# Kernel tuning notes

Measured on AMD Instinct MI355X. Metric: run time of the kernel, lower is better.

Reference implementation:

```python
import jax, jax.numpy as jnp
import numpy as np

C_S, C_Z, H = 384, 128, 8
HD = C_S // H
EPS = 1e-5

def _layernorm(x, g, b):
    mu = jnp.mean(x, axis=-1, keepdims=True)
    var = jnp.mean((x - mu) ** 2, axis=-1, keepdims=True)
    return (x - mu) * jax.lax.rsqrt(var + EPS) * g + b

def setup_inputs() -> dict:
    key = jax.random.key(0)
    ks = jax.random.split(key, 12)
    B, L = 1, 768
    sc = lambda d: 1.0 / np.sqrt(d)
    return {
        "single": jax.random.normal(ks[0], (B, L, C_S), jnp.float32),
        "pair": jax.random.normal(ks[1], (B, L, L, C_Z), jnp.float32),
        "g_s": jnp.ones((C_S,), jnp.float32),
        "b_s": jnp.zeros((C_S,), jnp.float32),
        "g_z": jnp.ones((C_Z,), jnp.float32),
        "b_z": jnp.zeros((C_Z,), jnp.float32),
        "Wq": jax.random.normal(ks[2], (C_S, C_S), jnp.float32) * sc(C_S),
        "Wk": jax.random.normal(ks[3], (C_S, C_S), jnp.float32) * sc(C_S),
        "Wv": jax.random.normal(ks[4], (C_S, C_S), jnp.float32) * sc(C_S),
        "Wb": jax.random.normal(ks[5], (C_Z, H), jnp.float32) * sc(C_Z),
        "Wo": jax.random.normal(ks[6], (C_S, C_S), jnp.float32) * sc(C_S),
        "bo": jnp.zeros((C_S,), jnp.float32),
        "Wg": jax.random.normal(ks[7], (C_S, C_S), jnp.float32) * sc(C_S),
        "bg": jnp.zeros((C_S,), jnp.float32),
    }

def reference(single, pair, g_s, b_s, g_z, b_z, Wq, Wk, Wv, Wb, Wo, bo, Wg, bg):
    B, L, _ = single.shape
    s = _layernorm(single, g_s, b_s)                      # [B,L,C_S]
    z = _layernorm(pair, g_z, b_z)                        # [B,L,L,C_Z]
    q = (s @ Wq.T).reshape(B, L, H, HD)
    k = (s @ Wk.T).reshape(B, L, H, HD)
    v = (s @ Wv.T).reshape(B, L, H, HD)
    attn = jnp.einsum('bihd,bjhd->bhij', q, k) / np.sqrt(HD)
    bias = jnp.einsum('bijz,zh->bhij', z, Wb)             # pair bias per head
    attn = jax.nn.softmax(attn + bias, axis=-1)
    out = jnp.einsum('bhij,bjhd->bihd', attn, v).reshape(B, L, C_S)
    gate = jax.nn.sigmoid(s @ Wg.T + bg)
    return single + gate * (out @ Wo.T + bo)
```

## Files before the change

### kernel.cpp

```cpp
#include <hip/hip_runtime.h>
#include <hip/hip_bf16.h>
#include <cstdint>
#include <cstddef>

#define LSEQ 768
#define CS 384
#define CZ 128
#define NH 8
#define HD 48
#define LL (LSEQ*LSEQ)
#define WELEM 147456

static constexpr float EPS = 1e-5f;
static constexpr float QK_SCALE = 0.14433756729740643f;

typedef unsigned short u16;
typedef __attribute__((ext_vector_type(8))) short bf16x8;
typedef __attribute__((ext_vector_type(4))) float f32x4;

__device__ __forceinline__ u16 f2bf_s(float f){
  unsigned int u = __float_as_uint(f);
  unsigned int r = u + 0x7fffu + ((u >> 16) & 1u);
  return (u16)(r >> 16);
}

__global__ __launch_bounds__(256) void k_prep(
    const float* __restrict__ single,
    const float* __restrict__ g, const float* __restrict__ b,
    const float* __restrict__ Wq, const float* __restrict__ Wk,
    const float* __restrict__ Wv, const float* __restrict__ Wg,
    const float* __restrict__ Wo,
    u16* __restrict__ s_bf, u16* __restrict__ Wbf){
  const int blk = blockIdx.x;
  if(blk < 192){
    const int wave = threadIdx.x >> 6, lane = threadIdx.x & 63;
    const int i = blk*4 + wave;
    const float* row = single + i*CS;
    float x[6];
    float sum = 0.f;
#pragma unroll
    for(int e=0;e<6;e++){ x[e] = row[lane + 64*e]; sum += x[e]; }
#pragma unroll
    for(int m=32;m>=1;m>>=1) sum += __shfl_xor(sum, m, 64);
    const float mu = sum * (1.f/CS);
    float vs = 0.f;
#pragma unroll
    for(int e=0;e<6;e++){ float d = x[e]-mu; vs += d*d; }
#pragma unroll
    for(int m=32;m>=1;m>>=1) vs += __shfl_xor(vs, m, 64);
    const float rs = rsqrtf(vs*(1.f/CS) + EPS);
#pragma unroll
    for(int e=0;e<6;e++){
      int c = lane + 64*e;
      s_bf[i*CS + c] = f2bf_s((x[e]-mu)*rs*g[c] + b[c]);
    }
  } else {
    const int idx = (blk-192)*256 + threadIdx.x;
    const int which = idx / 36864;
    const int off = (idx - which*36864)*4;
    const float* src = (which==0)?Wq:(which==1)?Wk:(which==2)?Wv:(which==3)?Wg:Wo;
    const float4 u = *(const float4*)(src + off);
    ushort4 o;
    o.x = f2bf_s(u.x); o.y = f2bf_s(u.y); o.z = f2bf_s(u.z); o.w = f2bf_s(u.w);
    *(ushort4*)(Wbf + (size_t)which*WELEM + off) = o;
  }
}

#define NQKVG 288
#define NPAIR 3072
__global__ __launch_bounds__(256,4) void k_pair_qkvg(
    const float* __restrict__ pair,
    const float* __restrict__ g_z,
    const float* __restrict__ b_z,
    const float* __restrict__ Wb,
    float* __restrict__ bias,
    const u16* __restrict__ s_bf, const u16* __restrict__ Wbf,
    const float* __restrict__ bg,
    u16* __restrict__ qb, u16* __restrict__ kb,
    u16* __restrict__ vT, float* __restrict__ gate){
  const int t = threadIdx.x;
  const int lane = t & 63;

  if(blockIdx.x < NQKVG){
    const int blk = blockIdx.x;
    const int w = t >> 6, ln = lane & 15, quad = lane >> 4;
    const int bx = blk % 12, by = blk / 12;
    const int m0 = bx*64 + w*16;
    const int which = by / 6;
    const int n0 = (by % 6)*64;
    const u16* W = Wbf + (size_t)which*WELEM;

    const u16* arow = s_bf + (size_t)(m0+ln)*CS + quad*8;
    const u16* brow = W + (size_t)(n0+ln)*CS + quad*8;

    f32x4 acc[4];
#pragma unroll
    for(int nb=0;nb<4;nb++) acc[nb] = (f32x4){0.f,0.f,0.f,0.f};

#pragma unroll 2
    for(int k0=0;k0<CS;k0+=32){
      bf16x8 a = *(const bf16x8*)(arow + k0);
#pragma unroll
      for(int nb=0;nb<4;nb++){
        bf16x8 bb = *(const bf16x8*)(brow + (size_t)nb*16*CS + k0);
        acc[nb] = __builtin_amdgcn_mfma_f32_16x16x32_bf16(a, bb, acc[nb], 0,0,0);
      }
    }

    if(which == 2){
#pragma unroll
      for(int nb=0;nb<4;nb++){
        const int col = n0 + nb*16 + ln;
        ushort4 sv;
        sv.x = f2bf_s(acc[nb][0]); sv.y = f2bf_s(acc[nb][1]);
        sv.z = f2bf_s(acc[nb][2]); sv.w = f2bf_s(acc[nb][3]);
        *(ushort4*)(vT + (size_t)col*LSEQ + m0 + quad*4) = sv;
      }
    } else {
#pragma unroll
      for(int nb=0;nb<4;nb++){
#pragma unroll
        for(int r=0;r<4;r++){
          const int row = m0 + quad*4 + r;
          const int col = n0 + nb*16 + ln;
          const float val = acc[nb][r];
          if(which==0)      qb[row*CS+col] = f2bf_s(val*QK_SCALE);
          else if(which==1) kb[row*CS+col] = f2bf_s(val);
          else              gate[row*CS+col] = 1.f/(1.f + __expf(-(val + bg[col])));
        }
      }
    }
    return;
  }

  const int wave = t >> 6;
  const int sub  = lane >> 4;
  const int lg   = lane & 15;
  const int z0   = lg*8;

  float wb_r[64], gz[8], bz[8];
#pragma unroll
  for(int zz=0; zz<8; zz++){
    gz[zz] = g_z[z0+zz];
    bz[zz] = b_z[z0+zz];
#pragma unroll
    for(int h=0; h<NH; h++) wb_r[zz*8+h] = Wb[(z0+zz)*NH + h];
  }
  const int hmap = 4*(lg&1) + (lg&2) + ((lg>>2)&1);

  const int ngroups = LL/16;
  for(int gidx = blockIdx.x - NQKVG; gidx < ngroups; gidx += NPAIR){
    const int r = gidx*16 + wave*4 + sub;
    const float4 u0 = *(const float4*)(pair + (size_t)r*CZ + z0);
    const float4 u1 = *(const float4*)(pair + (size_t)r*CZ + z0 + 4);
    float x[8] = {u0.x,u0.y,u0.z,u0.w,u1.x,u1.y,u1.z,u1.w};
    float sum=0.f, sq=0.f;
#pragma unroll
    for(int e=0;e<8;e++){ sum += x[e]; sq += x[e]*x[e]; }
#pragma unroll
    for(int m=1;m<16;m<<=1){ sum += __shfl_xor(sum,m,64); sq += __shfl_xor(sq,m,64); }
    const float mu = sum*(1.f/CZ);
    const float rs = rsqrtf(sq*(1.f/CZ) - mu*mu + EPS);
    float acc[8];
#pragma unroll
    for(int h=0;h<8;h++) acc[h]=0.f;
#pragma unroll
    for(int e=0;e<8;e++){
      const float zn = (x[e]-mu)*rs*gz[e] + bz[e];
#pragma unroll
      for(int h=0;h<8;h++) acc[h] += zn*wb_r[e*8+h];
    }
    float k1[4];
    {
      const bool hi = lg & 1;
#pragma unroll
      for(int j=0;j<4;j++){
        float send = hi ? acc[j] : acc[j+4];
        float recv = __shfl_xor(send, 1, 64);
        k1[j] = (hi ? acc[j+4] : acc[j]) + recv;
      }
    }
    float k2[2];
    {
      const bool hi = lg & 2;
#pragma unroll
      for(int j=0;j<2;j++){
        float send = hi ? k1[j] : k1[j+2];
        float recv = __shfl_xor(send, 2, 64);
        k2[j] = (hi ? k1[j+2] : k1[j]) + recv;
      }
    }
    float k3;
    {
      const bool hi = lg & 4;
      float send = hi ? k2[0] : k2[1];
      float recv = __shfl_xor(send, 4, 64);
      k3 = (hi ? k2[1] : k2[0]) + recv;
    }
    k3 += __shfl_xor(k3, 8, 64);
    if(lg < 8) bias[(size_t)hmap*LL + r] = k3;
  }
}

__global__ __launch_bounds__(256) void k_flash(
    const u16* __restrict__ qb, const u16* __restrict__ kb,
    const u16* __restrict__ vT, const float* __restrict__ bias,
    u16* __restrict__ attno_bf){
  const int h  = blockIdx.y;
  const int i0 = blockIdx.x * 16;
  const int t  = threadIdx.x;
  const int w    = t >> 6;
  const int lane = t & 63;
  const int ln   = lane & 15;
  const int quad = lane >> 4;

  __shared__ u16  S_lds[4][16][32];
  __shared__ float O_lds[4][16][48];
  __shared__ float ml_lds[4][2][16];

  const bf16x8 zf = {0,0,0,0,0,0,0,0};

  bf16x8 aq0, aq1;
  {
    const u16* qrow = qb + (size_t)(i0 + ln)*CS + h*HD;
    aq0 = *(const bf16x8*)(qrow + quad*8);
    aq1 = (quad < 2) ? *(const bf16x8*)(qrow + 32 + quad*8) : zf;
  }

  float m_r[4], l_r[4];
  f32x4 o[3];
#pragma unroll
  for(int r=0;r<4;r++){ m_r[r] = -INFINITY; l_r[r] = 0.f; }
#pragma unroll
  for(int db=0;db<3;db++) o[db] = (f32x4){0.f,0.f,0.f,0.f};

  for(int jt=0; jt<6; jt++){
    const int j0 = w*192 + jt*32;
    f32x4 s_f[2];
#pragma unroll
    for(int jb=0;jb<2;jb++){
      const u16* krow = kb + (size_t)(j0 + jb*16 + ln)*CS + h*HD;
      bf16x8 bk0 = *(const bf16x8*)(krow + quad*8);
      bf16x8 bk1 = (quad < 2) ? *(const bf16x8*)(krow + 32 + quad*8) : zf;
      f32x4 acc = (f32x4){0.f,0.f,0.f,0.f};
      acc = __builtin_amdgcn_mfma_f32_16x16x32_bf16(aq0, bk0, acc, 0,0,0);
      acc = __builtin_amdgcn_mfma_f32_16x16x32_bf16(aq1, bk1, acc, 0,0,0);
      s_f[jb] = acc;
    }
    float sv[2][4];
#pragma unroll
    for(int jb=0;jb<2;jb++)
#pragma unroll
      for(int r=0;r<4;r++)
        sv[jb][r] = s_f[jb][r] +
          bias[(size_t)h*LL + (size_t)(i0 + quad*4 + r)*LSEQ + j0 + jb*16 + ln];
    float tmax[4];
#pragma unroll
    for(int r=0;r<4;r++) tmax[r] = fmaxf(sv[0][r], sv[1][r]);
#pragma unroll
    for(int r=0;r<4;r++)
#pragma unroll
      for(int m=1;m<16;m<<=1) tmax[r] = fmaxf(tmax[r], __shfl_xor(tmax[r], m, 64));
    float alpha[4];
#pragma unroll
    for(int r=0;r<4;r++){
      const float mn = fmaxf(m_r[r], tmax[r]);
      alpha[r] = __expf(m_r[r] - mn);
      m_r[r] = mn;
    }
    float p[2][4], tsum[4];
#pragma unroll
    for(int r=0;r<4;r++){
      p[0][r] = __expf(sv[0][r] - m_r[r]);
      p[1][r] = __expf(sv[1][r] - m_r[r]);
      tsum[r] = p[0][r] + p[1][r];
    }
#pragma unroll
    for(int r=0;r<4;r++)
#pragma unroll
      for(int m=1;m<16;m<<=1) tsum[r] += __shfl_xor(tsum[r], m, 64);
#pragma unroll
    for(int r=0;r<4;r++) l_r[r] = l_r[r]*alpha[r] + tsum[r];
#pragma unroll
    for(int db=0;db<3;db++)
#pragma unroll
      for(int r=0;r<4;r++) o[db][r] *= alpha[r];
#pragma unroll
    for(int jb=0;jb<2;jb++)
#pragma unroll
      for(int r=0;r<4;r++) S_lds[w][quad*4+r][jb*16+ln] = f2bf_s(p[jb][r]);
    bf16x8 ap = *(const bf16x8*)&S_lds[w][ln][quad*8];
#pragma unroll
    for(int db=0;db<3;db++){
      bf16x8 bv = *(const bf16x8*)(vT + (size_t)(h*HD + db*16 + ln)*LSEQ + j0 + quad*8);
      o[db] = __builtin_amdgcn_mfma_f32_16x16x32_bf16(ap, bv, o[db], 0,0,0);
    }
  }

#pragma unroll
  for(int db=0;db<3;db++)
#pragma unroll
    for(int r=0;r<4;r++) O_lds[w][quad*4+r][db*16+ln] = o[db][r];
  if(ln == 0){
#pragma unroll
    for(int r=0;r<4;r++){
      ml_lds[w][0][quad*4+r] = m_r[r];
      ml_lds[w][1][quad*4+r] = l_r[r];
    }
  }
  __syncthreads();
#pragma unroll
  for(int e=0;e<3;e++){
    const int idx = t + e*256;
    const int row = idx / 48, d = idx % 48;
    float M = ml_lds[0][0][row];
#pragma unroll
    for(int ww=1;ww<4;ww++) M = fmaxf(M, ml_lds[ww][0][row]);
    float L = 0.f, O = 0.f;
#pragma unroll
    for(int ww=0;ww<4;ww++){
      const float f = __expf(ml_lds[ww][0][row] - M);
      L += ml_lds[ww][1][row] * f;
      O += O_lds[ww][row][d] * f;
    }
    attno_bf[(size_t)(i0+row)*CS + h*HD + d] = f2bf_s(O / L);
  }
}

__global__ __launch_bounds__(256) void k_final(
    const u16* __restrict__ attno_bf, const u16* __restrict__ Wo_bf,
    const float* __restrict__ bo, const float* __restrict__ single,
    const float* __restrict__ gate, float* __restrict__ out){
  const int t = threadIdx.x;
  const int w = t >> 6, lane = t & 63, ln = lane & 15, quad = lane >> 4;
  const int m0 = blockIdx.x*64 + w*16;
  const int n0 = blockIdx.y*64;

  const u16* arow = attno_bf + (size_t)(m0+ln)*CS + quad*8;
  const u16* brow = Wo_bf + (size_t)(n0+ln)*CS + quad*8;

  f32x4 acc[4];
#pragma unroll
  for(int nb=0;nb<4;nb++) acc[nb] = (f32x4){0.f,0.f,0.f,0.f};

#pragma unroll 4
  for(int k0=0;k0<CS;k0+=32){
    bf16x8 a = *(const bf16x8*)(arow + k0);
#pragma unroll
    for(int nb=0;nb<4;nb++){
      bf16x8 bb = *(const bf16x8*)(brow + (size_t)nb*16*CS + k0);
      acc[nb] = __builtin_amdgcn_mfma_f32_16x16x32_bf16(a, bb, acc[nb], 0,0,0);
    }
  }
#pragma unroll
  for(int nb=0;nb<4;nb++){
#pragma unroll
    for(int r=0;r<4;r++){
      const int row = m0 + quad*4 + r;
      const int col = n0 + nb*16 + ln;
      const float val = acc[nb][r] + bo[col];
      out[row*CS+col] = single[row*CS+col] + gate[row*CS+col]*val;
    }
  }
}

extern "C" void kernel_launch(void* const* d_in, const int* in_sizes, int n_in,
                              void* d_out, int out_size, void* d_ws, size_t ws_size,
                              hipStream_t stream){
  (void)in_sizes; (void)n_in; (void)out_size; (void)ws_size;
  const float* single = (const float*)d_in[0];
  const float* pair   = (const float*)d_in[1];
  const float* g_s    = (const float*)d_in[2];
  const float* b_s    = (const float*)d_in[3];
  const float* g_z    = (const float*)d_in[4];
  const float* b_z    = (const float*)d_in[5];
  const float* Wq     = (const float*)d_in[6];
  const float* Wk     = (const float*)d_in[7];
  const float* Wv     = (const float*)d_in[8];
  const float* Wb     = (const float*)d_in[9];
  const float* Wo     = (const float*)d_in[10];
  const float* bo     = (const float*)d_in[11];
  const float* Wg     = (const float*)d_in[12];
  const float* bg     = (const float*)d_in[13];
  float* out = (float*)d_out;

  float* ws     = (float*)d_ws;
  float* bias   = ws;
  float* gate   = ws + 4718592;
  u16*   s_bf   = (u16*)(gate + 294912);
  u16*   qb     = s_bf + 294912;
  u16*   kb     = qb + 294912;
  u16*   vT     = kb + 294912;
  u16*   attno  = vT + 294912;
  u16*   Wbf    = attno + 294912;

  hipLaunchKernelGGL(k_prep,      dim3(912),        dim3(256), 0, stream,
                     single, g_s, b_s, Wq, Wk, Wv, Wg, Wo, s_bf, Wbf);
  hipLaunchKernelGGL(k_pair_qkvg, dim3(NQKVG+NPAIR), dim3(256), 0, stream,
                     pair, g_z, b_z, Wb, bias, s_bf, Wbf, bg, qb, kb, vT, gate);
  hipLaunchKernelGGL(k_flash,     dim3(48,8),       dim3(256), 0, stream, qb, kb, vT, bias, attno);
  hipLaunchKernelGGL(k_final,     dim3(12,6),       dim3(256), 0, stream,
                     attno, Wbf + (size_t)4*WELEM, bo, single, gate, out);
}
```

Measured before the change: 476.8 us.

## Fuse single layernorm and weight casts into the pair/QKVG kernel

Removes the separate k_prep launch. Each QKVG block now recomputes the single-row layernorm for its 64 rows into shared memory, and converts fp32 weights to bf16 on the fly inside the MFMA loop. Extra blocks cast Wo for the final kernel. This saves one launch and its serialization, at the cost of redundant layernorm work, repeated fp32 weight loads and conversions per block, and a 48KB LDS allocation that now applies to the pair blocks too, which may cut occupancy.

```diff
diff --git a/kernel.cpp b/kernel.cpp
--- a/kernel.cpp
+++ b/kernel.cpp
@@ -24,49 +24,8 @@
   return (u16)(r >> 16);
 }
 
-__global__ __launch_bounds__(256) void k_prep(
-    const float* __restrict__ single,
-    const float* __restrict__ g, const float* __restrict__ b,
-    const float* __restrict__ Wq, const float* __restrict__ Wk,
-    const float* __restrict__ Wv, const float* __restrict__ Wg,
-    const float* __restrict__ Wo,
-    u16* __restrict__ s_bf, u16* __restrict__ Wbf){
-  const int blk = blockIdx.x;
-  if(blk < 192){
-    const int wave = threadIdx.x >> 6, lane = threadIdx.x & 63;
-    const int i = blk*4 + wave;
-    const float* row = single + i*CS;
-    float x[6];
-    float sum = 0.f;
-#pragma unroll
-    for(int e=0;e<6;e++){ x[e] = row[lane + 64*e]; sum += x[e]; }
-#pragma unroll
-    for(int m=32;m>=1;m>>=1) sum += __shfl_xor(sum, m, 64);
-    const float mu = sum * (1.f/CS);
-    float vs = 0.f;
-#pragma unroll
-    for(int e=0;e<6;e++){ float d = x[e]-mu; vs += d*d; }
-#pragma unroll
-    for(int m=32;m>=1;m>>=1) vs += __shfl_xor(vs, m, 64);
-    const float rs = rsqrtf(vs*(1.f/CS) + EPS);
-#pragma unroll
-    for(int e=0;e<6;e++){
-      int c = lane + 64*e;
-      s_bf[i*CS + c] = f2bf_s((x[e]-mu)*rs*g[c] + b[c]);
-    }
-  } else {
-    const int idx = (blk-192)*256 + threadIdx.x;
-    const int which = idx / 36864;
-    const int off = (idx - which*36864)*4;
-    const float* src = (which==0)?Wq:(which==1)?Wk:(which==2)?Wv:(which==3)?Wg:Wo;
-    const float4 u = *(const float4*)(src + off);
-    ushort4 o;
-    o.x = f2bf_s(u.x); o.y = f2bf_s(u.y); o.z = f2bf_s(u.z); o.w = f2bf_s(u.w);
-    *(ushort4*)(Wbf + (size_t)which*WELEM + off) = o;
-  }
-}
-
 #define NQKVG 288
+#define NCAST 144
 #define NPAIR 3072
 __global__ __launch_bounds__(256,4) void k_pair_qkvg(
     const float* __restrict__ pair,
@@ -74,12 +33,20 @@
     const float* __restrict__ b_z,
     const float* __restrict__ Wb,
     float* __restrict__ bias,
-    const u16* __restrict__ s_bf, const u16* __restrict__ Wbf,
+    const float* __restrict__ single,
+    const float* __restrict__ g_s,
+    const float* __restrict__ b_s,
+    const float* __restrict__ Wq, const float* __restrict__ Wk,
+    const float* __restrict__ Wv, const float* __restrict__ Wg,
+    const float* __restrict__ Wo,
     const float* __restrict__ bg,
+    u16* __restrict__ Wbf_o,
     u16* __restrict__ qb, u16* __restrict__ kb,
     u16* __restrict__ vT, float* __restrict__ gate){
   const int t = threadIdx.x;
   const int lane = t & 63;
+
+  __shared__ u16 lds_s[64][384];
 
   if(blockIdx.x < NQKVG){
     const int blk = blockIdx.x;
@@ -88,10 +55,34 @@
     const int m0 = bx*64 + w*16;
     const int which = by / 6;
     const int n0 = (by % 6)*64;
-    const u16* W = Wbf + (size_t)which*WELEM;
-
-    const u16* arow = s_bf + (size_t)(m0+ln)*CS + quad*8;
-    const u16* brow = W + (size_t)(n0+ln)*CS + quad*8;
+    const float* Wf = (which==0)?Wq:(which==1)?Wk:(which==2)?Wv:Wg;
+
+#pragma unroll 1
+    for(int rr=0; rr<16; rr++){
+      const int gi = m0 + rr;
+      const float* row = single + (size_t)gi*CS;
+      float x[6];
+      float sum = 0.f;
+#pragma unroll
+      for(int e=0;e<6;e++){ x[e] = row[lane + 64*e]; sum += x[e]; }
+#pragma unroll
+      for(int m=32;m>=1;m>>=1) sum += __shfl_xor(sum, m, 64);
+      const float mu = sum * (1.f/CS);
+      float vs = 0.f;
+#pragma unroll
+      for(int e=0;e<6;e++){ float d = x[e]-mu; vs += d*d; }
+#pragma unroll
+      for(int m=32;m>=1;m>>=1) vs += __shfl_xor(vs, m, 64);
+      const float rs = rsqrtf(vs*(1.f/CS) + EPS);
+#pragma unroll
+      for(int e=0;e<6;e++){
+        int c = lane + 64*e;
+        lds_s[w*16 + rr][c] = f2bf_s((x[e]-mu)*rs*g_s[c] + b_s[c]);
+      }
+    }
+
+    const u16* arow = &lds_s[w*16 + ln][quad*8];
+    const float* browf = Wf + (size_t)(n0+ln)*CS + quad*8;
 
     f32x4 acc[4];
 #pragma unroll
@@ -102,7 +93,14 @@
       bf16x8 a = *(const bf16x8*)(arow + k0);
 #pragma unroll
       for(int nb=0;nb<4;nb++){
-        bf16x8 bb = *(const bf16x8*)(brow + (size_t)nb*16*CS + k0);
+        const float* bp = browf + (size_t)nb*16*CS + k0;
+        const float4 u0 = *(const float4*)(bp);
+        const float4 u1 = *(const float4*)(bp + 4);
+        bf16x8 bb;
+        bb[0] = (short)f2bf_s(u0.x); bb[1] = (short)f2bf_s(u0.y);
+        bb[2] = (short)f2bf_s(u0.z); bb[3] = (short)f2bf_s(u0.w);
+        bb[4] = (short)f2bf_s(u1.x); bb[5] = (short)f2bf_s(u1.y);
+        bb[6] = (short)f2bf_s(u1.z); bb[7] = (short)f2bf_s(u1.w);
         acc[nb] = __builtin_amdgcn_mfma_f32_16x16x32_bf16(a, bb, acc[nb], 0,0,0);
       }
     }
@@ -133,6 +131,16 @@
     return;
   }
 
+  if(blockIdx.x < NQKVG + NCAST){
+    const int idx = (blockIdx.x - NQKVG)*256 + t;
+    const int off = idx*4;
+    const float4 u = *(const float4*)(Wo + off);
+    ushort4 o;
+    o.x = f2bf_s(u.x); o.y = f2bf_s(u.y); o.z = f2bf_s(u.z); o.w = f2bf_s(u.w);
+    *(ushort4*)(Wbf_o + off) = o;
+    return;
+  }
+
   const int wave = t >> 6;
   const int sub  = lane >> 4;
   const int lg   = lane & 15;
@@ -149,7 +157,7 @@
   const int hmap = 4*(lg&1) + (lg&2) + ((lg>>2)&1);
 
   const int ngroups = LL/16;
-  for(int gidx = blockIdx.x - NQKVG; gidx < ngroups; gidx += NPAIR){
+  for(int gidx = blockIdx.x - (NQKVG+NCAST); gidx < ngroups; gidx += NPAIR){
     const int r = gidx*16 + wave*4 + sub;
     const float4 u0 = *(const float4*)(pair + (size_t)r*CZ + z0);
     const float4 u1 = *(const float4*)(pair + (size_t)r*CZ + z0 + 4);
@@ -393,12 +401,13 @@
   u16*   vT     = kb + 294912;
   u16*   attno  = vT + 294912;
   u16*   Wbf    = attno + 294912;
-
-  hipLaunchKernelGGL(k_prep,      dim3(912),        dim3(256), 0, stream,
-                     single, g_s, b_s, Wq, Wk, Wv, Wg, Wo, s_bf, Wbf);
-  hipLaunchKernelGGL(k_pair_qkvg, dim3(NQKVG+NPAIR), dim3(256), 0, stream,
-                     pair, g_z, b_z, Wb, bias, s_bf, Wbf, bg, qb, kb, vT, gate);
+  u16*   Wbf_o  = Wbf + (size_t)4*WELEM;
+
+  hipLaunchKernelGGL(k_pair_qkvg, dim3(NQKVG+NCAST+NPAIR), dim3(256), 0, stream,
+                     pair, g_z, b_z, Wb, bias,
+                     single, g_s, b_s, Wq, Wk, Wv, Wg, Wo, bg,
+                     Wbf_o, qb, kb, vT, gate);
   hipLaunchKernelGGL(k_flash,     dim3(48,8),       dim3(256), 0, stream, qb, kb, vT, bias, attno);
   hipLaunchKernelGGL(k_final,     dim3(12,6),       dim3(256), 0, stream,
-                     attno, Wbf + (size_t)4*WELEM, bo, single, gate, out);
+                     attno, Wbf_o, bo, single, gate, out);
 }
```

Result: no change. 478.9 us (+0.4%).
